# Performance work log

Hardware: AMD Instinct MI355X
Metric: run time of the kernel (lower is better)

## Reference

```python
import jax, jax.numpy as jnp
import numpy as np

N_HEAD = 16
N_EMBD = 1024

def setup_inputs() -> dict:
    key = jax.random.key(0)
    k1, k2, k3 = jax.random.split(key, 3)
    B, T, C = 4, 2048, N_EMBD
    x = jax.random.normal(k1, (B, T, C), dtype=jnp.float32)
    attention_mask = jnp.ones((B, T), dtype=jnp.int32)
    # nn.Linear(C, 3C, bias=False): y = x @ W_attn, stored as (C, 3C)
    W_attn = jax.random.normal(k2, (C, 3 * C), dtype=jnp.float32) * 0.02
    W_proj = jax.random.normal(k3, (C, C), dtype=jnp.float32) * 0.02
    return {"x": x, "attention_mask": attention_mask, "W_attn": W_attn, "W_proj": W_proj}

def reference(x, attention_mask, W_attn, W_proj):
    B, T, C = x.shape
    H = N_HEAD
    D = C // H
    qkv = x @ W_attn                                   # [B,T,3C]
    q, k, v = jnp.split(qkv, 3, axis=2)
    # [B,T,C] -> [B,H,T,D]
    q = q.reshape(B, T, H, D).transpose(0, 2, 1, 3)
    k = k.reshape(B, T, H, D).transpose(0, 2, 1, 3)
    v = v.reshape(B, T, H, D).transpose(0, 2, 1, 3)
    scale = 1.0 / jnp.sqrt(jnp.asarray(D, x.dtype))
    att = jnp.einsum('bhqd,bhkd->bhqk', q, k) * scale  # [B,H,T,T]
    causal = jnp.tril(jnp.ones((T, T), dtype=bool))    # [T,T]
    pad = attention_mask != 0                          # [B,T], key-side padding
    mask = causal[None, None, :, :] & pad[:, None, None, :]
    att = jnp.where(mask, att, -jnp.inf)
    att = jax.nn.softmax(att, axis=-1)
    # dropout=0.0 (eval): attn_dropout and resid_dropout are identity
    y = jnp.einsum('bhqk,bhkd->bhqd', att, v)          # [B,H,T,D]
    y = y.transpose(0, 2, 1, 3).reshape(B, T, C)
    return y @ W_proj
```

## Files before the change

kernel.cpp:

```cpp
#include <hip/hip_runtime.h>
#include <hip/hip_bf16.h>
#include <math.h>

#define TT 2048
#define CC 1024
#define C3 3072
#define MM 8192

typedef __attribute__((ext_vector_type(8))) short short8;
typedef __attribute__((ext_vector_type(4))) float f32x4;

__device__ __forceinline__ short bf16b(float x) {
  __hip_bfloat16 h = __float2bfloat16(x);
  return *reinterpret_cast<short*>(&h);
}

__device__ __forceinline__ unsigned cvtpk(float lo, float hi) {
  unsigned r;
  asm("v_cvt_pk_bf16_f32 %0, %1, %2" : "=v"(r) : "v"(lo), "v"(hi));
  return r;
}

__device__ __forceinline__ float exp2a(float x) {
  float r;
  asm("v_exp_f32 %0, %1" : "=v"(r) : "v"(x));
  return r;
}

__device__ __forceinline__ void gload16(const void* g, void* l) {
  __builtin_amdgcn_global_load_lds(
      (const __attribute__((address_space(1))) unsigned int*)g,
      (__attribute__((address_space(3))) unsigned int*)l, 16, 0, 0);
}

__global__ __launch_bounds__(256) void cvt_x(const float* __restrict__ in,
                                             short* __restrict__ out, int n) {
  int i = (blockIdx.x * 256 + threadIdx.x) * 8;
  if (i >= n) return;
  float4 a = *reinterpret_cast<const float4*>(in + i);
  float4 b = *reinterpret_cast<const float4*>(in + i + 4);
  short8 r;
  r[0] = bf16b(a.x); r[1] = bf16b(a.y); r[2] = bf16b(a.z); r[3] = bf16b(a.w);
  r[4] = bf16b(b.x); r[5] = bf16b(b.y); r[6] = bf16b(b.z); r[7] = bf16b(b.w);
  *reinterpret_cast<short8*>(out + i) = r;
}

__global__ __launch_bounds__(256) void cvt_t(const float* __restrict__ in,
                                             short* __restrict__ out, int R, int Cc,
                                             int limit, float scale) {
  __shared__ float t[32][33];
  int c0 = blockIdx.x * 32, r0 = blockIdx.y * 32;
  int tx = threadIdx.x & 31, ty = threadIdx.x >> 5;
#pragma unroll
  for (int i = 0; i < 4; ++i)
    t[ty + i * 8][tx] = in[(size_t)(r0 + ty + i * 8) * Cc + c0 + tx];
  __syncthreads();
#pragma unroll
  for (int i = 0; i < 4; ++i) {
    const int orow = c0 + ty + i * 8;
    const float f = (orow < limit) ? scale : 1.f;
    out[(size_t)orow * R + r0 + tx] = bf16b(t[tx][ty + i * 8] * f);
  }
}

__global__ __launch_bounds__(256) void mask_pack(const int* __restrict__ amask,
                                                 unsigned long long* __restrict__ kmask) {
  const int gw = blockIdx.x * 4 + (threadIdx.x >> 6);
  const int lane = threadIdx.x & 63;
  unsigned long long bits = __ballot(amask[gw * 64 + lane] != 0);
  if (lane == 0) kmask[gw] = bits;
}

__global__ __launch_bounds__(256) void vtrans(const short* __restrict__ qkv,
                                              short* __restrict__ vT) {
  __shared__ short tile[64][72];
  const int bh = blockIdx.y, b = bh >> 4, h = bh & 15;
  const int t0 = blockIdx.x * 64;
  const int tr = threadIdx.x >> 2, dc = (threadIdx.x & 3) * 16;
  const short* src = qkv + (size_t)(b * TT + t0 + tr) * C3 + 2 * CC + h * 64 + dc;
  *reinterpret_cast<short8*>(&tile[tr][dc]) = *reinterpret_cast<const short8*>(src);
  *reinterpret_cast<short8*>(&tile[tr][dc + 8]) = *reinterpret_cast<const short8*>(src + 8);
  __syncthreads();
  const int d = threadIdx.x >> 2, p0 = (threadIdx.x & 3) * 16;
  short8 o1, o2;
#pragma unroll
  for (int i = 0; i < 8; ++i) {
    int p = p0 + i;
    int tl = (p & 32) | (((p >> 2) & 1) << 4) | (((p >> 3) & 3) << 2) | (p & 3);
    o1[i] = tile[tl][d];
    p = p0 + 8 + i;
    tl = (p & 32) | (((p >> 2) & 1) << 4) | (((p >> 3) & 3) << 2) | (p & 3);
    o2[i] = tile[tl][d];
  }
  short* dst = vT + (size_t)(bh * 64 + d) * TT + t0 + p0;
  *reinterpret_cast<short8*>(dst) = o1;
  *reinterpret_cast<short8*>(dst + 8) = o2;
}

template <int OUT_BF16>
__global__ __launch_bounds__(256) void gemm_bt(const short* __restrict__ A,
                                               const short* __restrict__ Bt,
                                               void* __restrict__ Cout,
                                               int M, int N, int K) {
  __shared__ __align__(16) char Ls[3 * 16384];
  const int tid = threadIdx.x, lane = tid & 63, w = tid >> 6;
  const int g = lane >> 4, cw = lane & 15;

  const int nwg = gridDim.x * gridDim.y;
  const int lin = blockIdx.y * gridDim.x + blockIdx.x;
  const int swz = (lin & 7) * (nwg >> 3) + (lin >> 3);
  const int by = swz & 63, bx = swz >> 6;
  const int m0 = by * 128, n0 = bx * 128;
  const int wr = (w >> 1) * 64, wc = (w & 1) * 64;

  f32x4 acc[4][4];
#pragma unroll
  for (int i = 0; i < 4; ++i)
#pragma unroll
    for (int j = 0; j < 4; ++j) acc[i][j] = (f32x4){0.f, 0.f, 0.f, 0.f};

  const int sr = tid >> 2;
  const int sc = ((tid & 3) ^ (sr & 3)) << 3;
  const short* Asrc = A + (size_t)(m0 + sr) * K + sc;
  const short* Bsrc = Bt + (size_t)(n0 + sr) * K + sc;
  const size_t ustep = (size_t)64 * K;

  const int nt = K >> 5;

#define STAGE(kt, buf)                                                        \
  {                                                                           \
    char* dst_ = Ls + (buf) * 16384;                                          \
    const int k0_ = (kt) * 32;                                                \
    _Pragma("unroll")                                                         \
    for (int u = 0; u < 2; ++u) {                                             \
      gload16(Asrc + u * ustep + k0_, dst_ + u * 4096 + tid * 16);            \
      gload16(Bsrc + u * ustep + k0_, dst_ + 8192 + u * 4096 + tid * 16);     \
    }                                                                         \
  }

  STAGE(0, 0);
  STAGE(1, 1);
  STAGE(2, 2);

  const int szr = (g * 16) ^ ((cw & 3) << 4);

  int cur = 0;
#pragma unroll 1
  for (int t = 0; t < nt; ++t) {
    const int rem = nt - 1 - t;
    if (rem >= 2) {
      asm volatile("s_waitcnt vmcnt(8)" ::: "memory");
    } else if (rem == 1) {
      asm volatile("s_waitcnt vmcnt(4)" ::: "memory");
    } else {
      asm volatile("s_waitcnt vmcnt(0)" ::: "memory");
    }
    asm volatile("s_barrier" ::: "memory");

    const char* LA = Ls + cur * 16384;
    const char* LB = LA + 8192;
    short8 af[4], bf[4];
#pragma unroll
    for (int mt = 0; mt < 4; ++mt)
      af[mt] = *reinterpret_cast<const short8*>(LA + (wr + mt * 16 + cw) * 64 + szr);
#pragma unroll
    for (int ntn = 0; ntn < 4; ++ntn)
      bf[ntn] = *reinterpret_cast<const short8*>(LB + (wc + ntn * 16 + cw) * 64 + szr);
    __builtin_amdgcn_s_setprio(1);
#pragma unroll
    for (int mt = 0; mt < 4; ++mt)
#pragma unroll
      for (int ntn = 0; ntn < 4; ++ntn)
        acc[mt][ntn] = __builtin_amdgcn_mfma_f32_16x16x32_bf16(af[mt], bf[ntn], acc[mt][ntn], 0, 0, 0);
    __builtin_amdgcn_s_setprio(0);

    asm volatile("s_barrier" ::: "memory");
    if (t + 3 < nt) STAGE(t + 3, cur);
    cur = (cur == 2) ? 0 : cur + 1;
  }
#undef STAGE

#pragma unroll
  for (int mt = 0; mt < 4; ++mt)
#pragma unroll
    for (int ntn = 0; ntn < 4; ++ntn)
#pragma unroll
      for (int j = 0; j < 4; ++j) {
        int row = m0 + wr + mt * 16 + g * 4 + j;
        int col = n0 + wc + ntn * 16 + cw;
        if (OUT_BF16)
          ((short*)Cout)[(size_t)row * N + col] = bf16b(acc[mt][ntn][j]);
        else
          ((float*)Cout)[(size_t)row * N + col] = acc[mt][ntn][j];
      }
}

__global__ __launch_bounds__(256, 4) void attn_mfma(const short* __restrict__ qkv,
                                                    const short* __restrict__ vT,
                                                    const unsigned long long* __restrict__ kmask,
                                                    short* __restrict__ y) {
  __shared__ __align__(16) char Ks[2 * 8192];
  __shared__ __align__(16) char Vs[2 * 8192];
  __shared__ unsigned long long km[32];
  const int tid = threadIdx.x, lane = tid & 63;
  const int w = tid >> 6;
  const int g = lane >> 4, cw = lane & 15;

  const int lin = blockIdx.y * 16 + blockIdx.x;
  const int swz = (lin & 7) * 128 + (lin >> 3);
  const int bh = swz >> 4, pr = swz & 15;
  const int b = bh >> 4, h = bh & 15;

  const int xorm = (cw & 7) << 4;
  const int srow = w * 8 + (lane >> 3);
  const int scb = (((lane & 7) ^ ((lane >> 3) & 7)) << 4);

  if (tid < 32) km[tid] = kmask[b * 32 + tid];

  const char* ksrc = (const char*)qkv + ((size_t)(b * TT + srow) * C3 + CC + h * 64) * 2 + scb;
  const char* vsrc = (const char*)vT + ((size_t)(bh * 64 + srow) * TT) * 2 + scb;

  const int kro = cw * 128;
  const int sz0 = (g * 16) ^ xorm;
  const int sz1 = (64 + g * 16) ^ xorm;

#pragma unroll 1
  for (int part = 0; part < 2; ++part) {
    const int qt = part ? 31 - pr : pr;
    const int qw = qt * 64 + w * 16;

    short8 qf[2];
#pragma unroll
    for (int ks = 0; ks < 2; ++ks)
      qf[ks] = *reinterpret_cast<const short8*>(
          &qkv[(size_t)(b * TT + qw + cw) * C3 + h * 64 + ks * 32 + g * 8]);

    f32x4 o[4];
#pragma unroll
    for (int nd = 0; nd < 4; ++nd) o[nd] = (f32x4){0.f, 0.f, 0.f, 0.f};
    float ls = 0.f;

    const int niter = qt + 1;
    const char* kp = ksrc;
    const char* vp = vsrc;
#pragma unroll
    for (int u = 0; u < 2; ++u) {
      gload16(kp + (size_t)(u * 32) * (C3 * 2), Ks + u * 4096 + tid * 16);
      gload16(vp + (size_t)(u * 32) * (TT * 2), Vs + u * 4096 + tid * 16);
    }

#pragma unroll 1
    for (int t = 0; t < niter; ++t) {
      const int cur = t & 1;
      if (t + 1 < niter) {
        kp += (size_t)64 * (C3 * 2);
        vp += 128;
        char* dK = Ks + (cur ^ 1) * 8192;
        char* dV = Vs + (cur ^ 1) * 8192;
#pragma unroll
        for (int u = 0; u < 2; ++u) {
          gload16(kp + (size_t)(u * 32) * (C3 * 2), dK + u * 4096 + tid * 16);
          gload16(vp + (size_t)(u * 32) * (TT * 2), dV + u * 4096 + tid * 16);
        }
        asm volatile("s_waitcnt vmcnt(4)" ::: "memory");
      } else {
        asm volatile("s_waitcnt vmcnt(0)" ::: "memory");
      }
      asm volatile("s_barrier" ::: "memory");

      const int kbase = t * 64;
      if (kbase <= qw + 15) {
        const char* KB = Ks + cur * 8192;
        const char* VB = Vs + cur * 8192;

        f32x4 s[4];
        __builtin_amdgcn_s_setprio(1);
#pragma unroll
        for (int nt = 0; nt < 4; ++nt) {
          short8 kf0 = *reinterpret_cast<const short8*>(KB + nt * 2048 + kro + sz0);
          short8 kf1 = *reinterpret_cast<const short8*>(KB + nt * 2048 + kro + sz1);
          f32x4 z = (f32x4){0.f, 0.f, 0.f, 0.f};
          s[nt] = __builtin_amdgcn_mfma_f32_16x16x32_bf16(kf0, qf[0], z, 0, 0, 0);
          s[nt] = __builtin_amdgcn_mfma_f32_16x16x32_bf16(kf1, qf[1], s[nt], 0, 0, 0);
        }
        __builtin_amdgcn_s_setprio(0);

        const unsigned long long kb = km[t];
        if ((kbase + 63 > qw) || (kb != ~0ULL)) {
          const int q = qw + cw;
#pragma unroll
          for (int nt = 0; nt < 4; ++nt)
#pragma unroll
            for (int j = 0; j < 4; ++j) {
              const int kh = nt * 16 + g * 4 + j;
              const bool mok = (kb >> kh) & 1;
              if (!(mok && kbase + kh <= q)) s[nt][j] = -1e30f;
            }
        }

        float rs = 0.f;
#pragma unroll
        for (int nt = 0; nt < 4; ++nt)
#pragma unroll
          for (int j = 0; j < 4; ++j) {
            const float p = exp2a(s[nt][j]);
            s[nt][j] = p;
            rs += p;
          }
        ls += rs;

        short8 pa[2];
#pragma unroll
        for (int ks2 = 0; ks2 < 2; ++ks2) {
          union { unsigned u[4]; short8 s8; } pc;
          pc.u[0] = cvtpk(s[2 * ks2][0], s[2 * ks2][1]);
          pc.u[1] = cvtpk(s[2 * ks2][2], s[2 * ks2][3]);
          pc.u[2] = cvtpk(s[2 * ks2 + 1][0], s[2 * ks2 + 1][1]);
          pc.u[3] = cvtpk(s[2 * ks2 + 1][2], s[2 * ks2 + 1][3]);
          pa[ks2] = pc.s8;
        }

        __builtin_amdgcn_s_setprio(1);
#pragma unroll
        for (int ks2 = 0; ks2 < 2; ++ks2)
#pragma unroll
          for (int nd = 0; nd < 4; ++nd) {
            short8 vf = *reinterpret_cast<const short8*>(
                VB + nd * 2048 + kro + (ks2 ? sz1 : sz0));
            o[nd] = __builtin_amdgcn_mfma_f32_16x16x32_bf16(pa[ks2], vf, o[nd], 0, 0, 0);
          }
        __builtin_amdgcn_s_setprio(0);
      }
      asm volatile("s_barrier" ::: "memory");
    }

    ls += __shfl_xor(ls, 16);
    ls += __shfl_xor(ls, 32);
#pragma unroll
    for (int j = 0; j < 4; ++j) {
      const float lj = __shfl(ls, (lane & 48) | (g * 4 + j));
      const float inv = 1.f / lj;
      const int q = qw + g * 4 + j;
#pragma unroll
      for (int nd = 0; nd < 4; ++nd)
        y[(size_t)(b * TT + q) * CC + h * 64 + nd * 16 + cw] = bf16b(o[nd][j] * inv);
    }
  }
}

extern "C" void kernel_launch(void* const* d_in, const int* in_sizes, int n_in,
                              void* d_out, int out_size, void* d_ws, size_t ws_size,
                              hipStream_t stream) {
  const float* x      = (const float*)d_in[0];
  const int*   amask  = (const int*)d_in[1];
  const float* W_attn = (const float*)d_in[2];
  const float* W_proj = (const float*)d_in[3];

  char* ws = (char*)d_ws;
  short* xb  = (short*)(ws);
  short* Wta = (short*)(ws + 16777216);
  short* Wtp = (short*)(ws + 23068672);
  short* qkv = (short*)(ws + 25165824);
  short* y   = (short*)(ws + 75497472);
  short* vT  = (short*)(ws + 92274688);
  unsigned long long* kmask = (unsigned long long*)(ws + 109051904);

  const float SC = 0.18033688011112043f;

  cvt_x<<<MM * CC / (256 * 8), 256, 0, stream>>>(x, xb, MM * CC);
  {
    dim3 g(C3 / 32, CC / 32);
    cvt_t<<<g, 256, 0, stream>>>(W_attn, Wta, CC, C3, CC, SC);
  }
  {
    dim3 g(CC / 32, CC / 32);
    cvt_t<<<g, 256, 0, stream>>>(W_proj, Wtp, CC, CC, 0, 1.f);
  }
  mask_pack<<<32, 256, 0, stream>>>(amask, kmask);
  {
    dim3 g(C3 / 128, MM / 128);
    gemm_bt<1><<<g, 256, 0, stream>>>(xb, Wta, qkv, MM, C3, CC);
  }
  {
    dim3 g(TT / 64, 64);
    vtrans<<<g, 256, 0, stream>>>(qkv, vT);
  }
  {
    dim3 g(16, 64);
    attn_mfma<<<g, 256, 0, stream>>>(qkv, vT, kmask, y);
  }
  {
    dim3 g(CC / 128, MM / 128);
    gemm_bt<0><<<g, 256, 0, stream>>>(y, Wtp, (void*)d_out, MM, CC, CC);
  }
}
```

Measured before the change: 180.4 us.

## Switch GEMM to BK=64 double-buffered LDS pipeline and drop block swizzle

Changes the bf16 GEMM from a triple-buffered K-step of 32 to a double-buffered K-step of 64. Each stage now holds 32KB and the LDS XOR swizzle is widened to 8 chunks. This halves the number of barrier/waitcnt iterations and gives more MFMA work per sync, which is meant to cut synchronisation overhead. It also removes the L2-friendly block-index swizzle, which risks worse cache reuse, and the pipeline is one stage shallower.

```diff
diff --git a/kernel.cpp b/kernel.cpp
--- a/kernel.cpp
+++ b/kernel.cpp
@@ -102,15 +102,10 @@
                                                const short* __restrict__ Bt,
                                                void* __restrict__ Cout,
                                                int M, int N, int K) {
-  __shared__ __align__(16) char Ls[3 * 16384];
+  __shared__ __align__(16) char Ls[2 * 32768];
   const int tid = threadIdx.x, lane = tid & 63, w = tid >> 6;
   const int g = lane >> 4, cw = lane & 15;
-
-  const int nwg = gridDim.x * gridDim.y;
-  const int lin = blockIdx.y * gridDim.x + blockIdx.x;
-  const int swz = (lin & 7) * (nwg >> 3) + (lin >> 3);
-  const int by = swz & 63, bx = swz >> 6;
-  const int m0 = by * 128, n0 = bx * 128;
+  const int m0 = blockIdx.y * 128, n0 = blockIdx.x * 128;
   const int wr = (w >> 1) * 64, wc = (w & 1) * 64;
 
   f32x4 acc[4][4];
@@ -119,64 +114,64 @@
 #pragma unroll
     for (int j = 0; j < 4; ++j) acc[i][j] = (f32x4){0.f, 0.f, 0.f, 0.f};
 
-  const int sr = tid >> 2;
-  const int sc = ((tid & 3) ^ (sr & 3)) << 3;
+  const int sr = tid >> 3;
+  const int sc = ((tid & 7) ^ (sr & 7)) << 3;
   const short* Asrc = A + (size_t)(m0 + sr) * K + sc;
   const short* Bsrc = Bt + (size_t)(n0 + sr) * K + sc;
-  const size_t ustep = (size_t)64 * K;
-
-  const int nt = K >> 5;
+  const size_t ustep = (size_t)32 * K;
+
+  const int nt = K >> 6;
 
 #define STAGE(kt, buf)                                                        \
   {                                                                           \
-    char* dst_ = Ls + (buf) * 16384;                                          \
-    const int k0_ = (kt) * 32;                                                \
+    char* dst_ = Ls + (buf) * 32768;                                          \
+    const int k0_ = (kt) * 64;                                                \
     _Pragma("unroll")                                                         \
-    for (int u = 0; u < 2; ++u) {                                             \
+    for (int u = 0; u < 4; ++u)                                               \
       gload16(Asrc + u * ustep + k0_, dst_ + u * 4096 + tid * 16);            \
-      gload16(Bsrc + u * ustep + k0_, dst_ + 8192 + u * 4096 + tid * 16);     \
-    }                                                                         \
+    _Pragma("unroll")                                                         \
+    for (int u = 0; u < 4; ++u)                                               \
+      gload16(Bsrc + u * ustep + k0_, dst_ + 16384 + u * 4096 + tid * 16);    \
   }
 
   STAGE(0, 0);
   STAGE(1, 1);
-  STAGE(2, 2);
-
-  const int szr = (g * 16) ^ ((cw & 3) << 4);
-
-  int cur = 0;
+
+  const int xorm = (cw & 7) << 4;
+
 #pragma unroll 1
   for (int t = 0; t < nt; ++t) {
-    const int rem = nt - 1 - t;
-    if (rem >= 2) {
+    if (t + 1 < nt) {
       asm volatile("s_waitcnt vmcnt(8)" ::: "memory");
-    } else if (rem == 1) {
-      asm volatile("s_waitcnt vmcnt(4)" ::: "memory");
     } else {
       asm volatile("s_waitcnt vmcnt(0)" ::: "memory");
     }
     asm volatile("s_barrier" ::: "memory");
 
-    const char* LA = Ls + cur * 16384;
-    const char* LB = LA + 8192;
-    short8 af[4], bf[4];
-#pragma unroll
-    for (int mt = 0; mt < 4; ++mt)
-      af[mt] = *reinterpret_cast<const short8*>(LA + (wr + mt * 16 + cw) * 64 + szr);
-#pragma unroll
-    for (int ntn = 0; ntn < 4; ++ntn)
-      bf[ntn] = *reinterpret_cast<const short8*>(LB + (wc + ntn * 16 + cw) * 64 + szr);
-    __builtin_amdgcn_s_setprio(1);
-#pragma unroll
-    for (int mt = 0; mt < 4; ++mt)
+    const char* LA = Ls + (t & 1) * 32768;
+    const char* LB = LA + 16384;
+
+#pragma unroll
+    for (int ks = 0; ks < 2; ++ks) {
+      const int xo = (ks * 64 + g * 16) ^ xorm;
+      short8 af[4], bf[4];
+#pragma unroll
+      for (int mt = 0; mt < 4; ++mt)
+        af[mt] = *reinterpret_cast<const short8*>(LA + (wr + mt * 16 + cw) * 128 + xo);
 #pragma unroll
       for (int ntn = 0; ntn < 4; ++ntn)
-        acc[mt][ntn] = __builtin_amdgcn_mfma_f32_16x16x32_bf16(af[mt], bf[ntn], acc[mt][ntn], 0, 0, 0);
-    __builtin_amdgcn_s_setprio(0);
+        bf[ntn] = *reinterpret_cast<const short8*>(LB + (wc + ntn * 16 + cw) * 128 + xo);
+      __builtin_amdgcn_s_setprio(1);
+#pragma unroll
+      for (int mt = 0; mt < 4; ++mt)
+#pragma unroll
+        for (int ntn = 0; ntn < 4; ++ntn)
+          acc[mt][ntn] = __builtin_amdgcn_mfma_f32_16x16x32_bf16(af[mt], bf[ntn], acc[mt][ntn], 0, 0, 0);
+      __builtin_amdgcn_s_setprio(0);
+    }
 
     asm volatile("s_barrier" ::: "memory");
-    if (t + 3 < nt) STAGE(t + 3, cur);
-    cur = (cur == 2) ? 0 : cur + 1;
+    if (t + 2 < nt) STAGE(t + 2, t & 1);
   }
 #undef STAGE
 
```

Measured after the change: 163.1 us. 9.6% less time.
